# Kernel optimization log

Measured on AMD Instinct MI355X. Metric: run time of the kernel, lower is better.

The kernel has to match this reference:

```python
import jax, jax.numpy as jnp
import numpy as np

B, T, E, H, HD, FF = 2, 2048, 1024, 16, 64, 4096
LN_EPS = 1e-5


def _ln(x, g, b):
    mu = jnp.mean(x, axis=-1, keepdims=True)
    var = jnp.var(x, axis=-1, keepdims=True)
    return (x - mu) * jax.lax.rsqrt(var + LN_EPS) * g + b


def setup_inputs() -> dict:
    key = jax.random.key(0)
    ks = jax.random.split(key, 8)
    s = 0.02
    return {
        "x": jax.random.normal(ks[0], (B, T, E), jnp.float32),
        "Wq": jax.random.normal(ks[1], (H, E, HD), jnp.float32) * s,
        "Wk": jax.random.normal(ks[2], (H, E, HD), jnp.float32) * s,
        "Wv": jax.random.normal(ks[3], (H, E, HD), jnp.float32) * s,
        "Wproj": jax.random.normal(ks[4], (E, E), jnp.float32) * s,
        "bproj": jnp.zeros((E,), jnp.float32),
        "W1": jax.random.normal(ks[5], (E, FF), jnp.float32) * s,
        "b1": jnp.zeros((FF,), jnp.float32),
        "W2": jax.random.normal(ks[6], (FF, E), jnp.float32) * s,
        "b2": jnp.zeros((E,), jnp.float32),
        "g1": jnp.ones((E,), jnp.float32),
        "be1": jnp.zeros((E,), jnp.float32),
        "g2": jnp.ones((E,), jnp.float32),
        "be2": jnp.zeros((E,), jnp.float32),
    }


def reference(x, Wq, Wk, Wv, Wproj, bproj, W1, b1, W2, b2, g1, be1, g2, be2):
    # --- pre-LN multi-head causal self-attention (dropout = eval/identity) ---
    h = _ln(x, g1, be1)  # [B,T,E]
    q = jnp.einsum('btd,hde->bhte', h, Wq)  # [B,H,T,HD]
    k = jnp.einsum('btd,hde->bhte', h, Wk)
    v = jnp.einsum('btd,hde->bhte', h, Wv)
    # NOTE: original code scales by C**-0.5 where C = embedding_dim (not head_size)
    scale = E ** (-0.5)
    wei = jnp.einsum('bhqe,bhke->bhqk', q, k) * scale  # [B,H,T,T]
    causal = jnp.tril(jnp.ones((T, T), dtype=bool))
    wei = jnp.where(causal, wei, -jnp.inf)
    attn = jax.nn.softmax(wei, axis=-1)
    o = jnp.einsum('bhqk,bhke->bhqe', attn, v)  # [B,H,T,HD]
    o = o.transpose(0, 2, 1, 3).reshape(B, T, E)  # concat heads
    o = o @ Wproj + bproj
    x = x + o
    # --- ReLU FFN ---
    h2 = _ln(x, g2, be2)
    f = jax.nn.relu(h2 @ W1 + b1) @ W2 + b2
    return x + f
```

## Files before the change

### kernel.cpp

```cpp
#include <hip/hip_runtime.h>
#include <hip/hip_bf16.h>
#include <stdint.h>

#define T_SEQ 2048
#define E_DIM 1024
#define H_NUM 16
#define HD_DIM 64
#define FF_DIM 4096
#define B_NUM 2
#define N_TOK (B_NUM * T_SEQ)

typedef unsigned short ushort_t;
typedef __bf16 bf16x8 __attribute__((ext_vector_type(8)));
typedef float f32x4 __attribute__((ext_vector_type(4)));

__device__ __forceinline__ float bf2f(ushort_t u) {
    return __uint_as_float(((unsigned)u) << 16);
}
__device__ __forceinline__ ushort_t f2bf(float f) {
    unsigned u = __float_as_uint(f);
    u += 0x7fffu + ((u >> 16) & 1u);
    return (ushort_t)(u >> 16);
}
__device__ __forceinline__ float bflo(unsigned u) { return __uint_as_float(u << 16); }
__device__ __forceinline__ float bfhi(unsigned u) { return __uint_as_float(u & 0xffff0000u); }

__device__ __forceinline__ void async_copy16(const ushort_t* g, ushort_t* l) {
    __builtin_amdgcn_global_load_lds(
        (__attribute__((address_space(1))) uint32_t*)(ushort_t*)g,
        (__attribute__((address_space(3))) uint32_t*)l, 16, 0, 0);
}

__global__ __launch_bounds__(256) void ln_kernel(const float* __restrict__ x,
                                                 const float* __restrict__ g,
                                                 const float* __restrict__ be,
                                                 ushort_t* __restrict__ out) {
    __shared__ float red[8];
    const int row = blockIdx.x, tid = threadIdx.x;
    const float* xr = x + (size_t)row * E_DIM;
    float4 v = ((const float4*)xr)[tid];
    float s = v.x + v.y + v.z + v.w;
    float sq = v.x * v.x + v.y * v.y + v.z * v.z + v.w * v.w;
    for (int off = 32; off; off >>= 1) {
        s += __shfl_xor(s, off);
        sq += __shfl_xor(sq, off);
    }
    const int wid = tid >> 6, lane = tid & 63;
    if (lane == 0) { red[wid] = s; red[4 + wid] = sq; }
    __syncthreads();
    s = red[0] + red[1] + red[2] + red[3];
    sq = red[4] + red[5] + red[6] + red[7];
    const float mean = s * (1.0f / E_DIM);
    const float var = sq * (1.0f / E_DIM) - mean * mean;
    const float rstd = rsqrtf(var + 1e-5f);
    float4 gv = ((const float4*)g)[tid];
    float4 bv = ((const float4*)be)[tid];
    unsigned o0 = f2bf((v.x - mean) * rstd * gv.x + bv.x);
    unsigned o1 = f2bf((v.y - mean) * rstd * gv.y + bv.y);
    unsigned o2 = f2bf((v.z - mean) * rstd * gv.z + bv.z);
    unsigned o3 = f2bf((v.w - mean) * rstd * gv.w + bv.w);
    uint2 w;
    w.x = o0 | (o1 << 16);
    w.y = o2 | (o3 << 16);
    ((uint2*)(out + (size_t)row * E_DIM))[tid] = w;
}

__global__ __launch_bounds__(256) void reduce_ln_kernel(const ushort_t* __restrict__ p0,
                                                        const ushort_t* __restrict__ p1,
                                                        const float* __restrict__ x,
                                                        const float* __restrict__ bias,
                                                        const float* __restrict__ g,
                                                        const float* __restrict__ be,
                                                        float* __restrict__ x1,
                                                        ushort_t* __restrict__ h2) {
    __shared__ float red[8];
    const int row = blockIdx.x, tid = threadIdx.x;
    uint2 u0 = ((const uint2*)(p0 + (size_t)row * E_DIM))[tid];
    uint2 u1 = ((const uint2*)(p1 + (size_t)row * E_DIM))[tid];
    float4 xv = ((const float4*)(x + (size_t)row * E_DIM))[tid];
    float4 bv = ((const float4*)bias)[tid];
    float4 v;
    v.x = xv.x + bv.x + bflo(u0.x) + bflo(u1.x);
    v.y = xv.y + bv.y + bfhi(u0.x) + bfhi(u1.x);
    v.z = xv.z + bv.z + bflo(u0.y) + bflo(u1.y);
    v.w = xv.w + bv.w + bfhi(u0.y) + bfhi(u1.y);
    ((float4*)(x1 + (size_t)row * E_DIM))[tid] = v;
    float s = v.x + v.y + v.z + v.w;
    float sq = v.x * v.x + v.y * v.y + v.z * v.z + v.w * v.w;
    for (int off = 32; off; off >>= 1) {
        s += __shfl_xor(s, off);
        sq += __shfl_xor(sq, off);
    }
    const int wid = tid >> 6, lane = tid & 63;
    if (lane == 0) { red[wid] = s; red[4 + wid] = sq; }
    __syncthreads();
    s = red[0] + red[1] + red[2] + red[3];
    sq = red[4] + red[5] + red[6] + red[7];
    const float mean = s * (1.0f / E_DIM);
    const float var = sq * (1.0f / E_DIM) - mean * mean;
    const float rstd = rsqrtf(var + 1e-5f);
    float4 gv = ((const float4*)g)[tid];
    float4 ev = ((const float4*)be)[tid];
    unsigned o0 = f2bf((v.x - mean) * rstd * gv.x + ev.x);
    unsigned o1 = f2bf((v.y - mean) * rstd * gv.y + ev.y);
    unsigned o2 = f2bf((v.z - mean) * rstd * gv.z + ev.z);
    unsigned o3 = f2bf((v.w - mean) * rstd * gv.w + ev.w);
    uint2 w;
    w.x = o0 | (o1 << 16);
    w.y = o2 | (o3 << 16);
    ((uint2*)(h2 + (size_t)row * E_DIM))[tid] = w;
}

__global__ __launch_bounds__(256) void reduce_out_kernel(const ushort_t* __restrict__ p0,
                                                         const ushort_t* __restrict__ p1,
                                                         const float* __restrict__ x1,
                                                         const float* __restrict__ bias,
                                                         float* __restrict__ out) {
    const int row = blockIdx.x, tid = threadIdx.x;
    uint2 u0 = ((const uint2*)(p0 + (size_t)row * E_DIM))[tid];
    uint2 u1 = ((const uint2*)(p1 + (size_t)row * E_DIM))[tid];
    float4 xv = ((const float4*)(x1 + (size_t)row * E_DIM))[tid];
    float4 bv = ((const float4*)bias)[tid];
    float4 v;
    v.x = xv.x + bv.x + bflo(u0.x) + bflo(u1.x);
    v.y = xv.y + bv.y + bfhi(u0.x) + bfhi(u1.x);
    v.z = xv.z + bv.z + bflo(u0.y) + bflo(u1.y);
    v.w = xv.w + bv.w + bfhi(u0.y) + bfhi(u1.y);
    ((float4*)(out + (size_t)row * E_DIM))[tid] = v;
}

__global__ __launch_bounds__(256) void transpose_kernel(const float* __restrict__ in,
                                                        ushort_t* __restrict__ out,
                                                        int R, int C) {
    __shared__ ushort_t tile[32][33];
    const int c0 = blockIdx.x * 32, r0 = blockIdx.y * 32;
    const int tx = threadIdx.x, ty = threadIdx.y;
#pragma unroll
    for (int i = 0; i < 32; i += 8) tile[ty + i][tx] = f2bf(in[(size_t)(r0 + ty + i) * C + (c0 + tx)]);
    __syncthreads();
#pragma unroll
    for (int i = 0; i < 32; i += 8) out[(size_t)(c0 + ty + i) * R + (r0 + tx)] = tile[tx][ty + i];
}

__global__ __launch_bounds__(256) void transpose_qkv_kernel(const float* __restrict__ Wq,
                                                            const float* __restrict__ Wk,
                                                            const float* __restrict__ Wv,
                                                            ushort_t* __restrict__ outT) {
    __shared__ ushort_t tile[32][33];
    const int z = blockIdx.z, m = z >> 4, hh = z & 15;
    const float* in = ((m == 0) ? Wq : ((m == 1) ? Wk : Wv)) + (size_t)hh * E_DIM * HD_DIM;
    ushort_t* out = outT + (size_t)(m * E_DIM + hh * HD_DIM) * E_DIM;
    const int c0 = blockIdx.x * 32, r0 = blockIdx.y * 32;
    const int tx = threadIdx.x, ty = threadIdx.y;
#pragma unroll
    for (int i = 0; i < 32; i += 8) tile[ty + i][tx] = f2bf(in[(size_t)(r0 + ty + i) * HD_DIM + (c0 + tx)]);
    __syncthreads();
#pragma unroll
    for (int i = 0; i < 32; i += 8) out[(size_t)(c0 + ty + i) * E_DIM + (r0 + tx)] = tile[tx][ty + i];
}

template <int MODE, int BK>
__global__ __launch_bounds__(256) void gemm_bt(const ushort_t* __restrict__ A,
                                               const ushort_t* __restrict__ BT,
                                               const float* __restrict__ bias,
                                               const float* __restrict__ resid,
                                               void* __restrict__ C0,
                                               ushort_t* __restrict__ C1,
                                               ushort_t* __restrict__ C2,
                                               int M, int N, int K, int lda) {
    __shared__ __align__(16) ushort_t lds_a[2][128 * BK];
    __shared__ __align__(16) ushort_t lds_b[2][128 * BK];
    const int tid = threadIdx.x;
    const int id = blockIdx.y * gridDim.x + blockIdx.x;
    const int band = id & 7, within = id >> 3;
    const int rpb = gridDim.y >> 3;
    const int by = band * rpb + (within % rpb);
    const int bx = within / rpb;
    const int m0 = by * 128, n0 = bx * 128;
    const int koff = blockIdx.z * K;
    const int wave = tid >> 6, lane = tid & 63;
    const int wm = (wave >> 1) * 64, wn = (wave & 1) * 64;
    const int quad = lane >> 4, l16 = lane & 15;
    f32x4 acc[4][4] = {};

    const int nk = K / BK;
    auto stage = [&](int kt, int buf) {
        const int k0 = koff + kt * BK;
#pragma unroll
        for (int it = 0; it < BK / 16; ++it) {
            const int ci = it * 256 + tid;
            const int kk = ci >> 9;
            const int rem = ci & 511;
            const int r = rem >> 2, kc = rem & 3;
            const int gk = k0 + kk * 32 + kc * 8;
            async_copy16(A + (size_t)(m0 + r) * lda + gk, &lds_a[buf][ci * 8]);
            async_copy16(BT + (size_t)(n0 + r) * lda + gk, &lds_b[buf][ci * 8]);
        }
    };
    stage(0, 0);

#pragma unroll 1
    for (int kt = 0; kt < nk; ++kt) {
        __syncthreads();
        if (kt + 1 < nk) stage(kt + 1, (kt + 1) & 1);
        const ushort_t* la = lds_a[kt & 1];
        const ushort_t* lb = lds_b[kt & 1];
#pragma unroll
        for (int kk = 0; kk < BK / 32; ++kk) {
            const ushort_t* lak = la + kk * 4096;
            const ushort_t* lbk = lb + kk * 4096;
            bf16x8 af[4], bfr[4];
#pragma unroll
            for (int i = 0; i < 4; i++) af[i] = *(const bf16x8*)&lak[(wm + i * 16 + l16) * 32 + quad * 8];
#pragma unroll
            for (int i = 0; i < 4; i++) bfr[i] = *(const bf16x8*)&lbk[(wn + i * 16 + l16) * 32 + quad * 8];
#pragma unroll
            for (int im = 0; im < 4; im++)
#pragma unroll
                for (int in = 0; in < 4; in++)
                    acc[im][in] = __builtin_amdgcn_mfma_f32_16x16x32_bf16(af[im], bfr[in], acc[im][in], 0, 0, 0);
        }
    }

    ushort_t* pc = nullptr;
    if (MODE == 3) pc = (blockIdx.z == 0) ? (ushort_t*)C0 : C1;
#pragma unroll
    for (int im = 0; im < 4; im++) {
#pragma unroll
        for (int in = 0; in < 4; in++) {
            const int col = n0 + wn + in * 16 + l16;
            float bv = (MODE == 1 || MODE == 2) ? bias[col] : 0.0f;
#pragma unroll
            for (int r = 0; r < 4; r++) {
                const int row = m0 + wm + im * 16 + quad * 4 + r;
                float v = acc[im][in][r] + bv;
                if (MODE == 2) v = fmaxf(v, 0.0f);
                if (MODE == 1) v += resid[(size_t)row * N + col];
                if (MODE == 0) {
                    const int mat = col >> 10, c = col & 1023, hh = c >> 6, d = c & 63;
                    const int bb = row >> 11, tt = row & 2047;
                    const int bh = bb * H_NUM + hh;
                    size_t idx;
                    ushort_t* dst;
                    if (mat == 0) {
                        idx = ((((size_t)bh * 32 + (tt >> 6)) * 8 + (d >> 3)) * 64 + (tt & 63)) * 8 + (d & 7);
                        dst = (ushort_t*)C0;
                        v *= 0.0450842048f;
                    } else if (mat == 1) {
                        idx = ((((size_t)bh * 32 + (tt >> 6)) * 8 + (d >> 3)) * 64 + (tt & 63)) * 8 + (d & 7);
                        dst = C1;
                    } else {
                        idx = ((((size_t)bh * 32 + (tt >> 6)) * 8 + ((tt & 63) >> 3)) * 64 + d) * 8 + (tt & 7);
                        dst = C2;
                    }
                    dst[idx] = f2bf(v);
                } else if (MODE == 1) {
                    ((float*)C0)[(size_t)row * N + col] = v;
                } else if (MODE == 2) {
                    ((ushort_t*)C0)[(size_t)row * N + col] = f2bf(v);
                } else {
                    pc[(size_t)row * N + col] = f2bf(v);
                }
            }
        }
    }
    (void)M;
}

__global__ __launch_bounds__(256) void attn_flash(const ushort_t* __restrict__ qP,
                                                  const ushort_t* __restrict__ kP,
                                                  const ushort_t* __restrict__ vP,
                                                  ushort_t* __restrict__ o) {
    __shared__ __align__(16) ushort_t K_lds[2][4096];
    __shared__ __align__(16) ushort_t V_lds[2][4096];
    __shared__ __align__(16) ushort_t P_lds[4 * 16 * 72];
    const int h = blockIdx.x, p = blockIdx.y, b = blockIdx.z;
    const int bh = b * H_NUM + h;
    const int tid = threadIdx.x;
    const int wave = tid >> 6, lane = tid & 63;
    const int quad = lane >> 4, l16 = lane & 15;
    const int qrow0 = wave * 16;
    ushort_t* Pw = &P_lds[wave * 16 * 72];
    const ushort_t* kt_base = kP + (size_t)bh * 32 * 4096;
    const ushort_t* vt_base = vP + (size_t)bh * 32 * 4096;
    bf16x8 onesf;
#pragma unroll
    for (int j = 0; j < 8; ++j) onesf[j] = (__bf16)1.0f;

#pragma unroll 1
    for (int phase = 0; phase < 2; ++phase) {
        const int qt = (phase == 0) ? (31 - p) : p;
        const ushort_t* qbase = qP + ((size_t)bh * 32 + qt) * 4096;
        bf16x8 qf[2];
#pragma unroll
        for (int kk = 0; kk < 2; kk++)
            qf[kk] = *(const bf16x8*)&qbase[((kk * 4 + quad) * 64 + qrow0 + l16) * 8];
        f32x4 oacc[4] = {};
        f32x4 lacc = {};
        const int nkt = qt + 1;
        __syncthreads();
#pragma unroll
        for (int it = 0; it < 2; ++it) {
            const int ci = it * 256 + tid;
            async_copy16(kt_base + ci * 8, &K_lds[0][ci * 8]);
            async_copy16(vt_base + ci * 8, &V_lds[0][ci * 8]);
        }
#pragma unroll 1
        for (int kt = 0; kt < nkt; ++kt) {
            __syncthreads();
            if (kt + 1 < nkt) {
                const ushort_t* kn = kt_base + (size_t)(kt + 1) * 4096;
                const ushort_t* vn = vt_base + (size_t)(kt + 1) * 4096;
                ushort_t* kd = K_lds[(kt + 1) & 1];
                ushort_t* vd = V_lds[(kt + 1) & 1];
#pragma unroll
                for (int it = 0; it < 2; ++it) {
                    const int ci = it * 256 + tid;
                    async_copy16(kn + ci * 8, &kd[ci * 8]);
                    async_copy16(vn + ci * 8, &vd[ci * 8]);
                }
            }
            const ushort_t* Kb = K_lds[kt & 1];
            const ushort_t* Vb = V_lds[kt & 1];
            f32x4 sacc[4] = {};
#pragma unroll
            for (int kk = 0; kk < 2; kk++) {
                bf16x8 bfr[4];
#pragma unroll
                for (int in = 0; in < 4; in++)
                    bfr[in] = *(const bf16x8*)&Kb[(kk * 4 + quad) * 512 + (in * 16 + l16) * 8];
#pragma unroll
                for (int in = 0; in < 4; in++)
                    sacc[in] = __builtin_amdgcn_mfma_f32_16x16x32_bf16(qf[kk], bfr[in], sacc[in], 0, 0, 0);
            }
#pragma unroll
            for (int in = 0; in < 4; in++) {
                f32x4 sv = sacc[in];
                if (kt == qt) {
                    const int jc = in * 16 + l16;
#pragma unroll
                    for (int r = 0; r < 4; r++)
                        if (jc > qrow0 + quad * 4 + r) sv[r] = -3.0e38f;
                }
#pragma unroll
                for (int r = 0; r < 4; r++) {
                    const float e = exp2f(sv[r]);
                    Pw[(quad * 4 + r) * 72 + in * 16 + l16] =
                        (ushort_t)(__float_as_uint(e) >> 16);
                }
            }
#pragma unroll
            for (int kk = 0; kk < 2; kk++) {
                bf16x8 pf = *(const bf16x8*)&Pw[l16 * 72 + kk * 32 + quad * 8];
                lacc = __builtin_amdgcn_mfma_f32_16x16x32_bf16(pf, onesf, lacc, 0, 0, 0);
#pragma unroll
                for (int in = 0; in < 4; in++) {
                    bf16x8 vf = *(const bf16x8*)&Vb[(kk * 4 + quad) * 512 + (in * 16 + l16) * 8];
                    oacc[in] = __builtin_amdgcn_mfma_f32_16x16x32_bf16(pf, vf, oacc[in], 0, 0, 0);
                }
            }
        }
#pragma unroll
        for (int r = 0; r < 4; r++) {
            const float inv = 1.0f / lacc[r];
            const int trow = qt * 64 + qrow0 + quad * 4 + r;
#pragma unroll
            for (int in = 0; in < 4; in++) {
                o[(size_t)(b * T_SEQ + trow) * E_DIM + h * HD_DIM + in * 16 + l16] =
                    f2bf(oacc[in][r] * inv);
            }
        }
    }
}

extern "C" void kernel_launch(void* const* d_in, const int* in_sizes, int n_in,
                              void* d_out, int out_size, void* d_ws, size_t ws_size,
                              hipStream_t stream) {
    const float* x = (const float*)d_in[0];
    const float* Wq = (const float*)d_in[1];
    const float* Wk = (const float*)d_in[2];
    const float* Wv = (const float*)d_in[3];
    const float* Wproj = (const float*)d_in[4];
    const float* bproj = (const float*)d_in[5];
    const float* W1 = (const float*)d_in[6];
    const float* b1 = (const float*)d_in[7];
    const float* W2 = (const float*)d_in[8];
    const float* b2 = (const float*)d_in[9];
    const float* g1 = (const float*)d_in[10];
    const float* be1 = (const float*)d_in[11];
    const float* g2 = (const float*)d_in[12];
    const float* be2 = (const float*)d_in[13];

    char* ws = (char*)d_ws;
    const size_t MB = 1024 * 1024;
    ushort_t* W2T    = (ushort_t*)(ws + 0 * MB);
    float*    x1     = (float*)   (ws + 8 * MB);
    ushort_t* W1T    = (ushort_t*)(ws + 24 * MB);
    ushort_t* WprojT = (ushort_t*)(ws + 32 * MB);
    ushort_t* hln    = (ushort_t*)(ws + 34 * MB);
    ushort_t* ocat   = hln;
    ushort_t* WqkvT  = (ushort_t*)(ws + 42 * MB);
    ushort_t* qP     = (ushort_t*)(ws + 48 * MB);
    ushort_t* kP     = (ushort_t*)(ws + 56 * MB);
    ushort_t* vP     = (ushort_t*)(ws + 64 * MB);
    ushort_t* h2     = (ushort_t*)(ws + 72 * MB);
    ushort_t* f1     = (ushort_t*)(ws + 34 * MB);
    ushort_t* pp0    = (ushort_t*)(ws + 48 * MB);
    ushort_t* pp1    = (ushort_t*)(ws + 56 * MB);
    ushort_t* fp0    = (ushort_t*)(ws + 66 * MB);
    ushort_t* fp1    = (ushort_t*)(ws + 24 * MB);
    (void)ws_size; (void)in_sizes; (void)n_in; (void)out_size;

    const dim3 tb(32, 8, 1);
    transpose_qkv_kernel<<<dim3(2, 32, 48), tb, 0, stream>>>(Wq, Wk, Wv, WqkvT);
    transpose_kernel<<<dim3(32, 32, 1), tb, 0, stream>>>(Wproj, WprojT, E_DIM, E_DIM);
    transpose_kernel<<<dim3(128, 32, 1), tb, 0, stream>>>(W1, W1T, E_DIM, FF_DIM);
    transpose_kernel<<<dim3(32, 128, 1), tb, 0, stream>>>(W2, W2T, FF_DIM, E_DIM);

    ln_kernel<<<N_TOK, 256, 0, stream>>>(x, g1, be1, hln);
    gemm_bt<0, 32><<<dim3(24, 32), 256, 0, stream>>>(hln, WqkvT, nullptr, nullptr,
                                                     qP, kP, vP, N_TOK, 3 * E_DIM, E_DIM, E_DIM);
    attn_flash<<<dim3(16, 16, 2), 256, 0, stream>>>(qP, kP, vP, ocat);
    gemm_bt<3, 64><<<dim3(8, 32, 2), 256, 0, stream>>>(ocat, WprojT, nullptr, nullptr,
                                                       pp0, pp1, nullptr, N_TOK, E_DIM, 512, E_DIM);
    reduce_ln_kernel<<<N_TOK, 256, 0, stream>>>(pp0, pp1, x, bproj, g2, be2, x1, h2);
    gemm_bt<2, 64><<<dim3(32, 32), 256, 0, stream>>>(h2, W1T, b1, nullptr,
                                                     f1, nullptr, nullptr, N_TOK, FF_DIM, E_DIM, E_DIM);
    gemm_bt<3, 64><<<dim3(8, 32, 2), 256, 0, stream>>>(f1, W2T, nullptr, nullptr,
                                                       fp0, fp1, nullptr, N_TOK, E_DIM, 2048, FF_DIM);
    reduce_out_kernel<<<N_TOK, 256, 0, stream>>>(fp0, fp1, x1, b2, (float*)d_out);
}
```

Before: 336.0 us.

## Process both causal query tiles concurrently with 32-row tiles per wave

```diff
diff --git a/kernel.cpp b/kernel.cpp
--- a/kernel.cpp
+++ b/kernel.cpp
@@ -273,56 +273,58 @@
                                                   ushort_t* __restrict__ o) {
     __shared__ __align__(16) ushort_t K_lds[2][4096];
     __shared__ __align__(16) ushort_t V_lds[2][4096];
-    __shared__ __align__(16) ushort_t P_lds[4 * 16 * 72];
+    __shared__ __align__(16) ushort_t P_lds[4 * 32 * 72];
     const int h = blockIdx.x, p = blockIdx.y, b = blockIdx.z;
     const int bh = b * H_NUM + h;
     const int tid = threadIdx.x;
     const int wave = tid >> 6, lane = tid & 63;
     const int quad = lane >> 4, l16 = lane & 15;
-    const int qrow0 = wave * 16;
-    ushort_t* Pw = &P_lds[wave * 16 * 72];
+    const int w32 = wave & 1;
+    const int qt = (wave >> 1) ? p : (31 - p);
+    const int nkt = qt + 1;
+    const int nbar = 32 - p;
+    ushort_t* Pw = &P_lds[wave * 32 * 72];
     const ushort_t* kt_base = kP + (size_t)bh * 32 * 4096;
     const ushort_t* vt_base = vP + (size_t)bh * 32 * 4096;
     bf16x8 onesf;
 #pragma unroll
     for (int j = 0; j < 8; ++j) onesf[j] = (__bf16)1.0f;
 
+    const ushort_t* qbase = qP + ((size_t)bh * 32 + qt) * 4096;
+    bf16x8 qf[2][2];
+#pragma unroll
+    for (int im = 0; im < 2; im++)
+#pragma unroll
+        for (int kk = 0; kk < 2; kk++)
+            qf[im][kk] = *(const bf16x8*)&qbase[((kk * 4 + quad) * 64 + w32 * 32 + im * 16 + l16) * 8];
+    f32x4 oacc[2][4] = {};
+    f32x4 lacc[2] = {};
+
+#pragma unroll
+    for (int it = 0; it < 2; ++it) {
+        const int ci = it * 256 + tid;
+        async_copy16(kt_base + ci * 8, &K_lds[0][ci * 8]);
+        async_copy16(vt_base + ci * 8, &V_lds[0][ci * 8]);
+    }
 #pragma unroll 1
-    for (int phase = 0; phase < 2; ++phase) {
-        const int qt = (phase == 0) ? (31 - p) : p;
-        const ushort_t* qbase = qP + ((size_t)bh * 32 + qt) * 4096;
-        bf16x8 qf[2];
-#pragma unroll
-        for (int kk = 0; kk < 2; kk++)
-            qf[kk] = *(const bf16x8*)&qbase[((kk * 4 + quad) * 64 + qrow0 + l16) * 8];
-        f32x4 oacc[4] = {};
-        f32x4 lacc = {};
-        const int nkt = qt + 1;
+    for (int kt = 0; kt < nbar; ++kt) {
         __syncthreads();
-#pragma unroll
-        for (int it = 0; it < 2; ++it) {
-            const int ci = it * 256 + tid;
-            async_copy16(kt_base + ci * 8, &K_lds[0][ci * 8]);
-            async_copy16(vt_base + ci * 8, &V_lds[0][ci * 8]);
-        }
-#pragma unroll 1
-        for (int kt = 0; kt < nkt; ++kt) {
-            __syncthreads();
-            if (kt + 1 < nkt) {
-                const ushort_t* kn = kt_base + (size_t)(kt + 1) * 4096;
-                const ushort_t* vn = vt_base + (size_t)(kt + 1) * 4096;
-                ushort_t* kd = K_lds[(kt + 1) & 1];
-                ushort_t* vd = V_lds[(kt + 1) & 1];
-#pragma unroll
-                for (int it = 0; it < 2; ++it) {
-                    const int ci = it * 256 + tid;
-                    async_copy16(kn + ci * 8, &kd[ci * 8]);
-                    async_copy16(vn + ci * 8, &vd[ci * 8]);
-                }
-            }
+        if (kt + 1 < nbar) {
+            const ushort_t* kn = kt_base + (size_t)(kt + 1) * 4096;
+            const ushort_t* vn = vt_base + (size_t)(kt + 1) * 4096;
+            ushort_t* kd = K_lds[(kt + 1) & 1];
+            ushort_t* vd = V_lds[(kt + 1) & 1];
+#pragma unroll
+            for (int it = 0; it < 2; ++it) {
+                const int ci = it * 256 + tid;
+                async_copy16(kn + ci * 8, &kd[ci * 8]);
+                async_copy16(vn + ci * 8, &vd[ci * 8]);
+            }
+        }
+        if (kt < nkt) {
             const ushort_t* Kb = K_lds[kt & 1];
             const ushort_t* Vb = V_lds[kt & 1];
-            f32x4 sacc[4] = {};
+            f32x4 sacc[2][4] = {};
 #pragma unroll
             for (int kk = 0; kk < 2; kk++) {
                 bf16x8 bfr[4];
@@ -330,44 +332,59 @@
                 for (int in = 0; in < 4; in++)
                     bfr[in] = *(const bf16x8*)&Kb[(kk * 4 + quad) * 512 + (in * 16 + l16) * 8];
 #pragma unroll
-                for (int in = 0; in < 4; in++)
-                    sacc[in] = __builtin_amdgcn_mfma_f32_16x16x32_bf16(qf[kk], bfr[in], sacc[in], 0, 0, 0);
-            }
-#pragma unroll
-            for (int in = 0; in < 4; in++) {
-                f32x4 sv = sacc[in];
-                if (kt == qt) {
-                    const int jc = in * 16 + l16;
-#pragma unroll
-                    for (int r = 0; r < 4; r++)
-                        if (jc > qrow0 + quad * 4 + r) sv[r] = -3.0e38f;
+                for (int im = 0; im < 2; im++)
+#pragma unroll
+                    for (int in = 0; in < 4; in++)
+                        sacc[im][in] = __builtin_amdgcn_mfma_f32_16x16x32_bf16(qf[im][kk], bfr[in], sacc[im][in], 0, 0, 0);
+            }
+#pragma unroll
+            for (int im = 0; im < 2; im++) {
+#pragma unroll
+                for (int in = 0; in < 4; in++) {
+                    f32x4 sv = sacc[im][in];
+                    if (kt == qt) {
+                        const int jc = in * 16 + l16;
+                        const int rl = w32 * 32 + im * 16 + quad * 4;
+#pragma unroll
+                        for (int r = 0; r < 4; r++)
+                            if (jc > rl + r) sv[r] = -3.0e38f;
+                    }
+#pragma unroll
+                    for (int r = 0; r < 4; r++) {
+                        const float e = exp2f(sv[r]);
+                        Pw[(im * 16 + quad * 4 + r) * 72 + in * 16 + l16] =
+                            (ushort_t)(__float_as_uint(e) >> 16);
+                    }
                 }
-#pragma unroll
-                for (int r = 0; r < 4; r++) {
-                    const float e = exp2f(sv[r]);
-                    Pw[(quad * 4 + r) * 72 + in * 16 + l16] =
-                        (ushort_t)(__float_as_uint(e) >> 16);
+            }
+#pragma unroll
+            for (int kk = 0; kk < 2; kk++) {
+                bf16x8 pf[2];
+#pragma unroll
+                for (int im = 0; im < 2; im++) {
+                    pf[im] = *(const bf16x8*)&Pw[(im * 16 + l16) * 72 + kk * 32 + quad * 8];
+                    lacc[im] = __builtin_amdgcn_mfma_f32_16x16x32_bf16(pf[im], onesf, lacc[im], 0, 0, 0);
                 }
-            }
-#pragma unroll
-            for (int kk = 0; kk < 2; kk++) {
-                bf16x8 pf = *(const bf16x8*)&Pw[l16 * 72 + kk * 32 + quad * 8];
-                lacc = __builtin_amdgcn_mfma_f32_16x16x32_bf16(pf, onesf, lacc, 0, 0, 0);
 #pragma unroll
                 for (int in = 0; in < 4; in++) {
                     bf16x8 vf = *(const bf16x8*)&Vb[(kk * 4 + quad) * 512 + (in * 16 + l16) * 8];
-                    oacc[in] = __builtin_amdgcn_mfma_f32_16x16x32_bf16(pf, vf, oacc[in], 0, 0, 0);
+#pragma unroll
+                    for (int im = 0; im < 2; im++)
+                        oacc[im][in] = __builtin_amdgcn_mfma_f32_16x16x32_bf16(pf[im], vf, oacc[im][in], 0, 0, 0);
                 }
             }
         }
+    }
+#pragma unroll
+    for (int im = 0; im < 2; im++) {
 #pragma unroll
         for (int r = 0; r < 4; r++) {
-            const float inv = 1.0f / lacc[r];
-            const int trow = qt * 64 + qrow0 + quad * 4 + r;
+            const float inv = 1.0f / lacc[im][r];
+            const int trow = qt * 64 + w32 * 32 + im * 16 + quad * 4 + r;
 #pragma unroll
             for (int in = 0; in < 4; in++) {
                 o[(size_t)(b * T_SEQ + trow) * E_DIM + h * HD_DIM + in * 16 + l16] =
-                    f2bf(oacc[in][r] * inv);
+                    f2bf(oacc[im][in][r] * inv);
             }
         }
     }
```

Measured after the change: 361.0 us. +7.4%, slower.
